# Optimization experiments

Measured on AMD Instinct MI355X. Metric: run time of the kernel, lower is better.

## Reference

```python
import jax, jax.numpy as jnp
import numpy as np

N, I, H = 32, 64, 128
B, T = 16, 256


def setup_inputs() -> dict:
    key = jax.random.key(0)
    k1, k2, k3, k4, k5 = jax.random.split(key, 5)
    stdv = 1.0 / np.sqrt(H)
    x = jax.random.normal(k1, (B, T, N * I), dtype=jnp.float32)
    h0 = jnp.zeros((1, B, N * H), dtype=jnp.float32)
    c0 = jnp.zeros((1, B, N * H), dtype=jnp.float32)
    # Block-diagonal weights stored as batched per-block matrices.
    # weight_ih block i is [4H, I], weight_hh block i is [4H, H].
    weight_ih = jax.random.uniform(k2, (N, 4 * H, I), jnp.float32, -stdv, stdv)
    weight_hh = jax.random.uniform(k3, (N, 4 * H, H), jnp.float32, -stdv, stdv)
    bias_ih = jax.random.uniform(k4, (N, 4 * H), jnp.float32, -stdv, stdv)
    bias_hh = jax.random.uniform(k5, (N, 4 * H), jnp.float32, -stdv, stdv)
    return {"x": x, "h0": h0, "c0": c0, "weight_ih": weight_ih,
            "weight_hh": weight_hh, "bias_ih": bias_ih, "bias_hh": bias_hh}


def _wide_lstm(x, h0, c0, weight_ih, weight_hh, bias_ih, bias_hh):
    b, t, _ = x.shape
    xb = x.reshape(b, t, N, I)
    # Precompute input-to-gate projections for all timesteps: [B,T,N,4H]
    gates_x = jnp.einsum('btni,ngi->btng', xb, weight_ih) + bias_ih
    h_t = h0[0].reshape(b, N, H)
    c_t = c0[0].reshape(b, N, H)

    def step(carry, gx_t):
        h, c = carry
        gates_h = jnp.einsum('bnh,ngh->bng', h, weight_hh) + bias_hh
        gates = gx_t + gates_h  # [B,N,4H]
        i_g = jax.nn.sigmoid(gates[..., 0 * H:1 * H])
        f_g = jax.nn.sigmoid(gates[..., 1 * H:2 * H])
        g_g = jnp.tanh(gates[..., 2 * H:3 * H])
        o_g = jax.nn.sigmoid(gates[..., 3 * H:4 * H])
        c_new = f_g * c + i_g * g_g
        h_new = o_g * jnp.tanh(c_new)
        return (h_new, c_new), h_new

    (h_n, c_n), outs = jax.lax.scan(step, (h_t, c_t),
                                    jnp.swapaxes(gates_x, 0, 1))  # scan over T
    output = jnp.swapaxes(outs, 0, 1).reshape(b, t, N * H)
    return output, h_n.reshape(1, b, N * H), c_n.reshape(1, b, N * H)


def reference(x, h0, c0, weight_ih, weight_hh, bias_ih, bias_hh):
    return _wide_lstm(x, h0, c0, weight_ih, weight_hh, bias_ih, bias_hh)
```

## Files before the change

kernel.cpp:

```cpp
#include <hip/hip_runtime.h>
#include <hip/hip_bf16.h>
#include <cstdint>
#include <cstddef>


#define TSTEPS 256

typedef float  f32x4  __attribute__((ext_vector_type(4)));
typedef float  f32x2  __attribute__((ext_vector_type(2)));
typedef __bf16 bf16x8 __attribute__((ext_vector_type(8)));
typedef short  s16x8  __attribute__((ext_vector_type(8)));

union Frag { s16x8 s; bf16x8 b; };

#define KSIG -1.4426950408889634f
#define KTAN  2.8853900817779268f

__device__ __forceinline__ short f2bf(float f) {
  uint32_t u = __builtin_bit_cast(uint32_t, f);
  u += 0x7fffu + ((u >> 16) & 1u);
  return (short)(u >> 16);
}

__device__ __forceinline__ void sync_lds() {
  asm volatile("s_waitcnt lgkmcnt(0)" ::: "memory");
  __builtin_amdgcn_s_barrier();
  asm volatile("" ::: "memory");
}

__device__ __forceinline__ float sig2(float z) {
  return __builtin_amdgcn_rcpf(1.f + __builtin_amdgcn_exp2f(z));
}

__device__ __forceinline__ f32x4 mf(const Frag a, const Frag bb, f32x4 c) {
  return __builtin_amdgcn_mfma_f32_16x16x32_bf16(a.b, bb.b, c, 0, 0, 0);
}

__global__ __launch_bounds__(1024, 4) void wide_lstm(
    const float* __restrict__ x,   const float* __restrict__ h0,
    const float* __restrict__ c0,  const float* __restrict__ wih,
    const float* __restrict__ whh, const float* __restrict__ bih,
    const float* __restrict__ bhh, float* __restrict__ out)
{
  const int n     = blockIdx.x & 31;
  const int bg    = blockIdx.x >> 5;
  const int tid   = threadIdx.x;
  const int wv    = tid >> 6;
  const int lane  = tid & 63;
  const int col   = lane & 15;
  const int quad  = lane >> 4;
  const int b4    = col & 3;
  const int e2    = col >> 2;
  const int tsel  = e2 >> 1;
  const int hbase = 8 * wv;
  const int hl    = hbase + quad + 4 * tsel;
  const int b     = 4 * bg + b4;
  const bool wr   = ((e2 & 1) == 0);

  __shared__ alignas(16) short hbuf[2][4 * 144];
  __shared__ alignas(16) short xbuf[2][4 * 96];

  Frag wfr[6][2];
#pragma unroll
  for (int T = 0; T < 2; ++T) {
    const int g = 128 * (col & 3) + hbase + 4 * T + (col >> 2);
#pragma unroll
    for (int s = 0; s < 6; ++s) {
      const int k0 = 32 * s + quad * 8;
      const float* p = (s < 2) ? (wih + (size_t)(n * 512 + g) * 64  + k0)
                               : (whh + (size_t)(n * 512 + g) * 128 + (k0 - 64));
      const f32x4 lo = *(const f32x4*)p;
      const f32x4 hi = *(const f32x4*)(p + 4);
      Frag f;
      f.s[0]=f2bf(lo[0]); f.s[1]=f2bf(lo[1]); f.s[2]=f2bf(lo[2]); f.s[3]=f2bf(lo[3]);
      f.s[4]=f2bf(hi[0]); f.s[5]=f2bf(hi[1]); f.s[6]=f2bf(hi[2]); f.s[7]=f2bf(hi[3]);
      wfr[s][T] = f;
    }
  }

  f32x4 cb[2];
#pragma unroll
  for (int T = 0; T < 2; ++T) {
#pragma unroll
    for (int r = 0; r < 4; ++r) {
      const int g = n * 512 + 128 * r + hbase + 4 * T + quad;
      cb[T][r] = bih[g] + bhh[g];
    }
  }

  if (tid < 256) {
    const int bi = tid >> 6, j2 = (tid & 63) * 2;
    const f32x2 hv = *(const f32x2*)(h0 + (size_t)(4 * bg + bi) * 4096 + n * 128 + j2);
    *(uint32_t*)&hbuf[0][bi * 144 + j2] =
        (uint32_t)(uint16_t)f2bf(hv[0]) | ((uint32_t)(uint16_t)f2bf(hv[1]) << 16);
  }
  const int sxoff = ((tid >> 6) & 3) * 96 + (tid & 63);
  float xr = 0.f;
  const float* xnext = nullptr;
  if (tid < 256) {
    const int bq = tid >> 6, kq = tid & 63;
    const float* xp = x + (size_t)(4 * bg + bq) * (TSTEPS * 2048) + n * 64 + kq;
    xbuf[1][bq * 96 + kq] = f2bf(xp[2048]);
    xr = xp[2 * 2048];
    xnext = xp + 3 * 2048;
  }
  float cg = c0[(size_t)b * 4096 + n * 128 + hl];

  f32x4 acpre[2];
  {
    const float* q = x + (size_t)b * (TSTEPS * 2048) + n * 64 + 8 * quad;
    const f32x4 a0 = *(const f32x4*)q;
    const f32x4 a1 = *(const f32x4*)(q + 4);
    const f32x4 a2 = *(const f32x4*)(q + 32);
    const f32x4 a3 = *(const f32x4*)(q + 36);
    Frag xf0, xf1;
#pragma unroll
    for (int r = 0; r < 4; ++r) {
      xf0.s[r]     = f2bf(a0[r]);
      xf0.s[4 + r] = f2bf(a1[r]);
      xf1.s[r]     = f2bf(a2[r]);
      xf1.s[4 + r] = f2bf(a3[r]);
    }
#pragma unroll
    for (int T = 0; T < 2; ++T)
      acpre[T] = mf(wfr[1][T], xf1, mf(wfr[0][T], xf0, cb[T]));
  }
  __syncthreads();

  const int hoff  = b4 * 144 + quad * 8;
  const int xoff  = b4 * 96  + quad * 8;
  const int hwoff = b4 * 144 + hl;
  float* outp = out + (size_t)b * (TSTEPS * 4096) + n * 128 + hl;
  float ho = 0.f;
  const f32x4 kzero = (f32x4){0.f, 0.f, 0.f, 0.f};

#define LSTM_STEP(CUR, NXT, S)                                               \
  {                                                                          \
    Frag hf0, hf1, hf2, hf3, xg0, xg1;                                       \
    hf0.s = *(const s16x8*)&hbuf[CUR][hoff];                                 \
    hf1.s = *(const s16x8*)&hbuf[CUR][hoff + 32];                            \
    hf2.s = *(const s16x8*)&hbuf[CUR][hoff + 64];                            \
    hf3.s = *(const s16x8*)&hbuf[CUR][hoff + 96];                            \
    xg0.s = *(const s16x8*)&xbuf[NXT][xoff];                                 \
    xg1.s = *(const s16x8*)&xbuf[NXT][xoff + 32];                            \
    if (tid < 256) {                                                         \
      xbuf[CUR][sxoff] = f2bf(xr);                                           \
      if ((S) + 3 < TSTEPS) { xr = *xnext; xnext += 2048; }                  \
    }                                                                        \
    f32x4 ac1[2], ac2[2];                                                    \
    _Pragma("unroll") for (int T = 0; T < 2; ++T) {                          \
      ac1[T] = mf(wfr[3][T], hf1, mf(wfr[2][T], hf0, acpre[T]));             \
      ac2[T] = mf(wfr[5][T], hf3, mf(wfr[4][T], hf2, kzero));                \
    }                                                                        \
    _Pragma("unroll") for (int T = 0; T < 2; ++T)                            \
      acpre[T] = mf(wfr[1][T], xg1, mf(wfr[0][T], xg0, cb[T]));              \
    const f32x4 ps = tsel ? (ac1[1] + ac2[1]) : (ac1[0] + ac2[0]);           \
    const float si = sig2(KSIG * ps[0]);                                     \
    const float sf = sig2(KSIG * ps[1]);                                     \
    const float sg = sig2(KTAN * ps[2]);                                     \
    const float so = sig2(KSIG * ps[3]);                                     \
    float cn = __builtin_fmaf(sf, cg, si);                                   \
    cn = __builtin_fmaf(-2.f, si * sg, cn);                                  \
    cg = cn;                                                                 \
    ho = so * __builtin_fmaf(-2.f, sig2(KTAN * cn), 1.f);                    \
    if (wr) {                                                                \
      hbuf[NXT][hwoff] = f2bf(ho);                                           \
      *outp = ho;                                                            \
    }                                                                        \
    outp += 4096;                                                            \
    sync_lds();                                                              \
  }

  for (int t = 0; t < TSTEPS; t += 2) {
    LSTM_STEP(0, 1, t);
    LSTM_STEP(1, 0, t + 1);
  }
#undef LSTM_STEP

  if (wr) {
    out[16777216 +         (size_t)b * 4096 + n * 128 + hl] = ho;
    out[16777216 + 65536 + (size_t)b * 4096 + n * 128 + hl] = cg;
  }
}

extern "C" void kernel_launch(void* const* d_in, const int* in_sizes, int n_in,
                              void* d_out, int out_size, void* d_ws, size_t ws_size,
                              hipStream_t stream) {
  const float* x   = (const float*)d_in[0];
  const float* h0  = (const float*)d_in[1];
  const float* c0  = (const float*)d_in[2];
  const float* wih = (const float*)d_in[3];
  const float* whh = (const float*)d_in[4];
  const float* bih = (const float*)d_in[5];
  const float* bhh = (const float*)d_in[6];
  float* out = (float*)d_out;
  wide_lstm<<<128, 1024, 0, stream>>>(x, h0, c0, wih, whh, bih, bhh, out);
}
```

Measured before the change: 301.8 us.

## Load x fragments per lane from global into registers, drop LDS staging buffer

Removes the shared-memory x staging buffer, in which 256 threads each loaded one scalar and stored bf16 to LDS. Instead, every lane now loads its own 8-element x fragments directly from global memory two steps ahead into double-buffered registers. The bf16 conversion now uses the native __bf16 cast instead of manual rounding. This cuts LDS traffic and the dependence of the x path on the barrier, at the cost of redundant global loads across waves and more registers per lane.

```diff
diff --git a/kernel.cpp b/kernel.cpp
--- a/kernel.cpp
+++ b/kernel.cpp
@@ -58,7 +58,6 @@
   const bool wr   = ((e2 & 1) == 0);
 
   __shared__ alignas(16) short hbuf[2][4 * 144];
-  __shared__ alignas(16) short xbuf[2][4 * 96];
 
   Frag wfr[6][2];
 #pragma unroll
@@ -94,32 +93,30 @@
     *(uint32_t*)&hbuf[0][bi * 144 + j2] =
         (uint32_t)(uint16_t)f2bf(hv[0]) | ((uint32_t)(uint16_t)f2bf(hv[1]) << 16);
   }
-  const int sxoff = ((tid >> 6) & 3) * 96 + (tid & 63);
-  float xr = 0.f;
-  const float* xnext = nullptr;
-  if (tid < 256) {
-    const int bq = tid >> 6, kq = tid & 63;
-    const float* xp = x + (size_t)(4 * bg + bq) * (TSTEPS * 2048) + n * 64 + kq;
-    xbuf[1][bq * 96 + kq] = f2bf(xp[2048]);
-    xr = xp[2 * 2048];
-    xnext = xp + 3 * 2048;
-  }
   float cg = c0[(size_t)b * 4096 + n * 128 + hl];
+
+  const float* xlane = x + (size_t)b * (TSTEPS * 2048) + n * 64 + 8 * quad;
+
+  f32x4 xsA0, xsA1, xsA2, xsA3, xsB0, xsB1, xsB2, xsB3;
+  {
+    const float* p = xlane + 2048;
+    xsB0 = *(const f32x4*)p;        xsB1 = *(const f32x4*)(p + 4);
+    xsB2 = *(const f32x4*)(p + 32); xsB3 = *(const f32x4*)(p + 36);
+  }
 
   f32x4 acpre[2];
   {
-    const float* q = x + (size_t)b * (TSTEPS * 2048) + n * 64 + 8 * quad;
-    const f32x4 a0 = *(const f32x4*)q;
-    const f32x4 a1 = *(const f32x4*)(q + 4);
-    const f32x4 a2 = *(const f32x4*)(q + 32);
-    const f32x4 a3 = *(const f32x4*)(q + 36);
+    const f32x4 a0 = *(const f32x4*)xlane;
+    const f32x4 a1 = *(const f32x4*)(xlane + 4);
+    const f32x4 a2 = *(const f32x4*)(xlane + 32);
+    const f32x4 a3 = *(const f32x4*)(xlane + 36);
     Frag xf0, xf1;
 #pragma unroll
     for (int r = 0; r < 4; ++r) {
-      xf0.s[r]     = f2bf(a0[r]);
-      xf0.s[4 + r] = f2bf(a1[r]);
-      xf1.s[r]     = f2bf(a2[r]);
-      xf1.s[4 + r] = f2bf(a3[r]);
+      xf0.b[r]     = (__bf16)a0[r];
+      xf0.b[4 + r] = (__bf16)a1[r];
+      xf1.b[r]     = (__bf16)a2[r];
+      xf1.b[4 + r] = (__bf16)a3[r];
     }
 #pragma unroll
     for (int T = 0; T < 2; ++T)
@@ -128,25 +125,31 @@
   __syncthreads();
 
   const int hoff  = b4 * 144 + quad * 8;
-  const int xoff  = b4 * 96  + quad * 8;
   const int hwoff = b4 * 144 + hl;
   float* outp = out + (size_t)b * (TSTEPS * 4096) + n * 128 + hl;
   float ho = 0.f;
   const f32x4 kzero = (f32x4){0.f, 0.f, 0.f, 0.f};
 
-#define LSTM_STEP(CUR, NXT, S)                                               \
+#define LSTM_STEP(CUR, NXT, S, XC0, XC1, XC2, XC3, XN0, XN1, XN2, XN3)       \
   {                                                                          \
-    Frag hf0, hf1, hf2, hf3, xg0, xg1;                                       \
+    {                                                                        \
+      const int tt = ((S) + 2 < TSTEPS) ? (S) + 2 : (TSTEPS - 1);            \
+      const float* p = xlane + (size_t)tt * 2048;                            \
+      XC0 = *(const f32x4*)p;        XC1 = *(const f32x4*)(p + 4);           \
+      XC2 = *(const f32x4*)(p + 32); XC3 = *(const f32x4*)(p + 36);          \
+    }                                                                        \
+    Frag xg0, xg1;                                                           \
+    _Pragma("unroll") for (int r = 0; r < 4; ++r) {                          \
+      xg0.b[r]     = (__bf16)XN0[r];                                         \
+      xg0.b[4 + r] = (__bf16)XN1[r];                                         \
+      xg1.b[r]     = (__bf16)XN2[r];                                         \
+      xg1.b[4 + r] = (__bf16)XN3[r];                                         \
+    }                                                                        \
+    Frag hf0, hf1, hf2, hf3;                                                 \
     hf0.s = *(const s16x8*)&hbuf[CUR][hoff];                                 \
     hf1.s = *(const s16x8*)&hbuf[CUR][hoff + 32];                            \
     hf2.s = *(const s16x8*)&hbuf[CUR][hoff + 64];                            \
     hf3.s = *(const s16x8*)&hbuf[CUR][hoff + 96];                            \
-    xg0.s = *(const s16x8*)&xbuf[NXT][xoff];                                 \
-    xg1.s = *(const s16x8*)&xbuf[NXT][xoff + 32];                            \
-    if (tid < 256) {                                                         \
-      xbuf[CUR][sxoff] = f2bf(xr);                                           \
-      if ((S) + 3 < TSTEPS) { xr = *xnext; xnext += 2048; }                  \
-    }                                                                        \
     f32x4 ac1[2], ac2[2];                                                    \
     _Pragma("unroll") for (int T = 0; T < 2; ++T) {                          \
       ac1[T] = mf(wfr[3][T], hf1, mf(wfr[2][T], hf0, acpre[T]));             \
@@ -172,8 +175,8 @@
   }
 
   for (int t = 0; t < TSTEPS; t += 2) {
-    LSTM_STEP(0, 1, t);
-    LSTM_STEP(1, 0, t + 1);
+    LSTM_STEP(0, 1, t,     xsA0, xsA1, xsA2, xsA3, xsB0, xsB1, xsB2, xsB3);
+    LSTM_STEP(1, 0, t + 1, xsB0, xsB1, xsB2, xsB3, xsA0, xsA1, xsA2, xsA3);
   }
 #undef LSTM_STEP
 
```

Result: slower. 594.0 us (+96.8%).
